# Kernel optimization log

Hardware: AMD Instinct MI355X
Metric: run time of the kernel (lower is better)

Reference implementation:

```python
import itertools
import jax, jax.numpy as jnp
import numpy as np

INIT_STD = 0.1
N_PTS = 1_000_000
PLANE_RES = 512
OUT_DIM = 3
RANK = 8
FEAT_DIM = 32
FEAT_RES = 128


def grid_sample(grid, pts):
    """Equivalent of plenoxels grid_sample_wrapper / torch F.grid_sample.

    grid: [C, *spatial] (d spatial dims, d in {2,3})
    pts:  [N, d] in [-1, 1]; pts[:, k] indexes spatial dim d-1-k (torch x->W, y->H convention)
    bilinear/trilinear interpolation, align_corners=True, zeros padding.
    Returns [N, C].
    """
    spatial = grid.shape[1:]
    d = len(spatial)
    # sizes ordered per-pts-coordinate (reversed spatial order, torch convention)
    sizes_f = jnp.asarray([spatial[d - 1 - k] for k in range(d)], dtype=pts.dtype)
    sizes_i = jnp.asarray([spatial[d - 1 - k] for k in range(d)], dtype=jnp.int32)
    u = (pts + 1.0) * 0.5 * (sizes_f - 1.0)  # unnormalized coords, align_corners=True
    lo = jnp.floor(u)
    frac = u - lo  # [N, d]
    lo = lo.astype(jnp.int32)
    out = jnp.zeros((pts.shape[0], grid.shape[0]), dtype=pts.dtype)
    for corner in itertools.product((0, 1), repeat=d):  # 4 or 8 corners, fixed small loop
        ca = jnp.asarray(corner, dtype=jnp.int32)
        idx = lo + ca  # [N, d]
        valid = jnp.all((idx >= 0) & (idx < sizes_i), axis=-1)  # zeros padding outside
        w = jnp.prod(jnp.where(ca.astype(bool), frac, 1.0 - frac), axis=-1)
        w = w * valid.astype(pts.dtype)
        idx_c = jnp.clip(idx, 0, sizes_i - 1)
        # map pts-coord k back to spatial dim d-1-k for the gather
        vals = grid[(slice(None),) + tuple(idx_c[:, d - 1 - j] for j in range(d))]  # [C, N]
        out = out + w[:, None] * vals.T
    return out


def setup_inputs() -> dict:
    key = jax.random.key(0)
    k1, k2, k3, k4, k5 = jax.random.split(key, 5)
    pts = jax.random.uniform(k1, (N_PTS, 3), minval=-1.0, maxval=1.0, dtype=jnp.float32)
    C = OUT_DIM * RANK
    plane0 = INIT_STD * jax.random.normal(k2, (C, PLANE_RES, PLANE_RES), dtype=jnp.float32)
    plane1 = INIT_STD * jax.random.normal(k3, (C, PLANE_RES, PLANE_RES), dtype=jnp.float32)
    plane2 = INIT_STD * jax.random.normal(k4, (C, PLANE_RES, PLANE_RES), dtype=jnp.float32)
    features = INIT_STD * jax.random.normal(k5, (FEAT_DIM, FEAT_RES, FEAT_RES, FEAT_RES), dtype=jnp.float32)
    return {"pts": pts, "plane0": plane0, "plane1": plane1, "plane2": plane2, "features": features}


def reference(pts, plane0, plane1, plane2, features):
    """LowrankLearnableHash.compute_features: 3 plane bilinear gathers, elementwise
    multiply across planes, sum over rank, then trilinear lookup in feature volume."""
    n = pts.shape[0]
    combs = ((0, 1), (0, 2), (1, 2))  # itertools.combinations(range(3), 2)
    prod = None
    for plane, comb in zip((plane0, plane1, plane2), combs):
        s = grid_sample(plane, pts[:, jnp.asarray(comb)]).reshape(n, OUT_DIM, RANK)
        prod = s if prod is None else prod * s
    interp = prod.sum(axis=-1)  # [N, 3] coordinates into feature volume
    return grid_sample(features, interp)  # [N, FEAT_DIM]
```

## Files before the change

### kernel.cpp

```cpp
#include <hip/hip_runtime.h>

typedef float v4f __attribute__((ext_vector_type(4)));
typedef unsigned short u16;
typedef u16 u16x8 __attribute__((ext_vector_type(8)));

constexpr int PR  = 512;
constexpr int CP  = 24;
constexpr int FD  = 32;
constexpr int FR  = 128;
constexpr int PSZ = PR * PR;
constexpr int NBUCK = 32768;
constexpr int FW  = 16;
constexpr int FW0 = 56;

__device__ inline u16 f2bf(float f) {
    unsigned u = __float_as_uint(f);
    return (u16)((u + 0x7fffu + ((u >> 16) & 1u)) >> 16);
}
__device__ inline float bf2f(u16 h) { return __uint_as_float((unsigned)h << 16); }

__global__ __launch_bounds__(256) void transpose_planes(
    const float* __restrict__ p0, const float* __restrict__ p1,
    const float* __restrict__ p2, u16* __restrict__ wsB)
{
    __shared__ float lds[CP][256];
    int b   = blockIdx.x;
    int p   = b >> 10;
    int rem = b & 1023;
    int y   = rem >> 1;
    int x0  = (rem & 1) << 8;
    const float* src = (p == 0) ? p0 : (p == 1) ? p1 : p2;
    int t = threadIdx.x;
    #pragma unroll
    for (int c = 0; c < CP; ++c)
        lds[c][t] = src[c * PSZ + y * PR + x0 + t];
    __syncthreads();
    int tex = y * PR + x0 + t;
    #pragma unroll
    for (int g = 0; g < 3; ++g) {
        u16x8 w;
        #pragma unroll
        for (int k = 0; k < 8; ++k) w[k] = f2bf(lds[g * 8 + k][t]);
        *(u16x8*)(wsB + ((size_t)(p * 3 + g) * PSZ + tex) * 8) = w;
    }
}

__global__ __launch_bounds__(256) void pack_feat(
    const float* __restrict__ feat, float* __restrict__ wsF)
{
    int t = blockIdx.x * 256 + threadIdx.x;
    int c = t & 31;
    int v = t >> 5;
    int x = v & 15, y = (v >> 4) & 15, z = v >> 8;
    wsF[(size_t)v * FD + c] =
        feat[(size_t)c * FR * FR * FR + (size_t)(z + FW0) * FR * FR
             + (y + FW0) * FR + (x + FW0)];
}

__global__ __launch_bounds__(256) void zero_hist(unsigned* __restrict__ hist)
{
    int t = blockIdx.x * 256 + threadIdx.x;
    v4f z = {0.f, 0.f, 0.f, 0.f};
    *(v4f*)(hist + t * 4) = z;
}

__device__ inline int cell5(float p) {
    int c = (int)floorf((p + 1.0f) * 16.0f);
    return min(max(c, 0), 31);
}
__device__ inline unsigned spread3(unsigned v) {
    return (v & 1u) | ((v & 2u) << 2) | ((v & 4u) << 4) | ((v & 8u) << 6) | ((v & 16u) << 8);
}
__device__ inline unsigned morton_key(float x, float y, float z) {
    return spread3((unsigned)cell5(x)) | (spread3((unsigned)cell5(y)) << 1)
         | (spread3((unsigned)cell5(z)) << 2);
}

__global__ __launch_bounds__(256) void bucket_hist(
    const float* __restrict__ pts, unsigned* __restrict__ hist, int n)
{
    int i = blockIdx.x * blockDim.x + threadIdx.x;
    if (i >= n) return;
    float x = pts[3 * i], y = pts[3 * i + 1], z = pts[3 * i + 2];
    atomicAdd(&hist[morton_key(x, y, z)], 1u);
}

__global__ __launch_bounds__(1024) void scan_offsets(
    const unsigned* __restrict__ hist, unsigned* __restrict__ cursor)
{
    __shared__ unsigned sums[1024];
    int t = threadIdx.x;
    const int base = t * (NBUCK / 1024);
    unsigned loc[NBUCK / 1024];
    unsigned s = 0;
    #pragma unroll
    for (int j = 0; j < NBUCK / 1024; ++j) { loc[j] = s; s += hist[base + j]; }
    sums[t] = s;
    __syncthreads();
    for (int off = 1; off < 1024; off <<= 1) {
        unsigned v = (t >= off) ? sums[t - off] : 0u;
        __syncthreads();
        sums[t] += v;
        __syncthreads();
    }
    unsigned blockbase = (t == 0) ? 0u : sums[t - 1];
    #pragma unroll
    for (int j = 0; j < NBUCK / 1024; ++j) cursor[base + j] = blockbase + loc[j];
}

__global__ __launch_bounds__(256) void scatter_pts(
    const float* __restrict__ pts, unsigned* __restrict__ cursor,
    v4f* __restrict__ sorted, unsigned* __restrict__ ord, int n)
{
    int i = blockIdx.x * blockDim.x + threadIdx.x;
    if (i >= n) return;
    float x = pts[3 * i], y = pts[3 * i + 1], z = pts[3 * i + 2];
    unsigned key = morton_key(x, y, z);
    unsigned pos = atomicAdd(&cursor[key], 1u);
    v4f v; v.x = x; v.y = y; v.z = z; v.w = 0.f;
    sorted[pos] = v;
    ord[pos] = (unsigned)i;
}

template <int G>
__global__ __launch_bounds__(256, 8) void lrh_interp_g(
    const v4f* __restrict__ sorted, const u16* __restrict__ wsB,
    float* __restrict__ itp, int n)
{
    int nwg = gridDim.x;
    int q = nwg >> 3, r = nwg & 7;
    int xcd = blockIdx.x & 7, j = blockIdx.x >> 3;
    int wg = (xcd < r ? xcd * (q + 1) : r * (q + 1) + (xcd - r) * q) + j;
    int i = wg * 256 + threadIdx.x;
    if (i >= n) return;

    v4f pt = __builtin_nontemporal_load(&sorted[i]);
    float cx[3] = {pt.x, pt.x, pt.y};
    float cy[3] = {pt.y, pt.z, pt.z};

    float pr[8] = {1.f, 1.f, 1.f, 1.f, 1.f, 1.f, 1.f, 1.f};
    #pragma unroll
    for (int p = 0; p < 3; ++p) {
        float ux = (cx[p] + 1.0f) * 0.5f * (float)(PR - 1);
        float uy = (cy[p] + 1.0f) * 0.5f * (float)(PR - 1);
        float lx = floorf(ux), ly = floorf(uy);
        float fx = ux - lx,   fy = uy - ly;
        int ix0 = (int)lx, iy0 = (int)ly;
        int ix1 = min(ix0 + 1, PR - 1);
        int iy1 = min(iy0 + 1, PR - 1);
        float wx0 = 1.f - fx, wx1 = fx;
        float wy0 = 1.f - fy, wy1 = fy;
        float w00 = wx0 * wy0, w01 = wx1 * wy0;
        float w10 = wx0 * wy1, w11 = wx1 * wy1;

        const u16* slab = wsB + (size_t)(p * 3 + G) * PSZ * 8;
        const u16x8 A = *(const u16x8*)(slab + (iy0 * PR + ix0) * 8);
        const u16x8 B = *(const u16x8*)(slab + (iy0 * PR + ix1) * 8);
        const u16x8 C = *(const u16x8*)(slab + (iy1 * PR + ix0) * 8);
        const u16x8 D = *(const u16x8*)(slab + (iy1 * PR + ix1) * 8);
        #pragma unroll
        for (int e = 0; e < 8; ++e) {
            float s = w00 * bf2f(A[e]) + w01 * bf2f(B[e])
                    + w10 * bf2f(C[e]) + w11 * bf2f(D[e]);
            pr[e] *= s;
        }
    }
    float itpv = ((pr[0] + pr[1]) + (pr[2] + pr[3]))
               + ((pr[4] + pr[5]) + (pr[6] + pr[7]));
    __builtin_nontemporal_store(itpv, &itp[i]);
}

__global__ __launch_bounds__(256) void lrh_feat(
    const float* __restrict__ itp0, const float* __restrict__ itp1,
    const float* __restrict__ itp2, const unsigned* __restrict__ ord,
    const float* __restrict__ wsF, const float* __restrict__ feat,
    float* __restrict__ out, int n)
{
    int t = blockIdx.x * blockDim.x + threadIdx.x;
    int i = t >> 3, e = t & 7;
    if (i >= n) return;
    float ip[3] = {itp0[i], itp1[i], itp2[i]};
    unsigned orig = ord[i];

    float fr[3];
    int   j0[3];
    bool inw = true;
    #pragma unroll
    for (int k = 0; k < 3; ++k) {
        float uu = (ip[k] + 1.0f) * 0.5f * (float)(FR - 1);
        float lf = floorf(uu);
        fr[k] = uu - lf;
        j0[k] = (int)lf;
        inw = inw && (j0[k] >= FW0) && (j0[k] + 1 <= FW0 + FW - 1);
    }

    v4f r = {0.f, 0.f, 0.f, 0.f};
    if (__builtin_expect(inw, 1)) {
        int lx = j0[0] - FW0, ly = j0[1] - FW0, lz = j0[2] - FW0;
        int base = ((lz * FW + ly) * FW + lx) * FD;
        float wx1 = fr[0], wx0 = 1.f - fr[0];
        float wy1 = fr[1], wy0 = 1.f - fr[1];
        float wz1 = fr[2], wz0 = 1.f - fr[2];
        #pragma unroll
        for (int m = 0; m < 8; ++m) {
            int bx = m & 1, by = (m >> 1) & 1, bz = m >> 2;
            int off = base + (bz * FW * FW + by * FW + bx) * FD;
            float w = (bx ? wx1 : wx0) * (by ? wy1 : wy0) * (bz ? wz1 : wz0);
            v4f f = *(const v4f*)(wsF + off + e * 4);
            #pragma unroll
            for (int c = 0; c < 4; ++c) r[c] = fmaf(w, f[c], r[c]);
        }
    } else {
        float v0[3], v1[3];
        int i0c[3], i1c[3];
        #pragma unroll
        for (int k = 0; k < 3; ++k) {
            int jj = j0[k];
            v0[k] = (jj   >= 0 && jj   < FR) ? 1.f : 0.f;
            v1[k] = (jj+1 >= 0 && jj+1 < FR) ? 1.f : 0.f;
            i0c[k] = min(max(jj,     0), FR - 1);
            i1c[k] = min(max(jj + 1, 0), FR - 1);
        }
        #pragma unroll
        for (int m = 0; m < 8; ++m) {
            int bx = m & 1, by = (m >> 1) & 1, bz = m >> 2;
            int xi = bx ? i1c[0] : i0c[0];
            int yi = by ? i1c[1] : i0c[1];
            int zi = bz ? i1c[2] : i0c[2];
            float w = (bx ? fr[0] * v1[0] : (1.f - fr[0]) * v0[0])
                    * (by ? fr[1] * v1[1] : (1.f - fr[1]) * v0[1])
                    * (bz ? fr[2] * v1[2] : (1.f - fr[2]) * v0[2]);
            int offc = zi * FR * FR + yi * FR + xi;
            #pragma unroll
            for (int c = 0; c < 4; ++c) {
                const float* Fc = feat + (size_t)(e * 4 + c) * (FR * FR * FR);
                r[c] = fmaf(w, Fc[offc], r[c]);
            }
        }
    }

    *(v4f*)(out + (size_t)orig * FD + e * 4) = r;
}

extern "C" void kernel_launch(void* const* d_in, const int* in_sizes, int n_in,
                              void* d_out, int out_size, void* d_ws, size_t ws_size,
                              hipStream_t stream) {
    const float* pts  = (const float*)d_in[0];
    const float* p0   = (const float*)d_in[1];
    const float* p1   = (const float*)d_in[2];
    const float* p2   = (const float*)d_in[3];
    const float* feat = (const float*)d_in[4];
    float* out = (float*)d_out;
    int n = in_sizes[0] / 3;

    size_t off = 0;
    auto alloc = [&](size_t sz) { size_t o = off; off = (off + sz + 255) & ~(size_t)255; return o; };
    const size_t off_trans  = alloc((size_t)3 * PSZ * CP * sizeof(u16));
    const size_t off_sorted = alloc((size_t)n * sizeof(v4f));
    const size_t off_hist   = alloc(NBUCK * sizeof(unsigned));
    const size_t off_cursor = alloc(NBUCK * sizeof(unsigned));
    const size_t off_ord    = alloc((size_t)n * sizeof(unsigned));
    const size_t off_itp0   = alloc((size_t)n * sizeof(float));
    const size_t off_itp1   = alloc((size_t)n * sizeof(float));
    const size_t off_itp2   = alloc((size_t)n * sizeof(float));
    const size_t off_featw  = alloc((size_t)FW * FW * FW * FD * sizeof(float));

    char* ws = (char*)d_ws;
    u16*      wsB     = (u16*)(ws + off_trans);
    v4f*      sorted  = (v4f*)(ws + off_sorted);
    unsigned* hist    = (unsigned*)(ws + off_hist);
    unsigned* cursor  = (unsigned*)(ws + off_cursor);
    unsigned* ord     = (unsigned*)(ws + off_ord);
    float*    itp0    = (float*)(ws + off_itp0);
    float*    itp1    = (float*)(ws + off_itp1);
    float*    itp2    = (float*)(ws + off_itp2);
    float*    wsF     = (float*)(ws + off_featw);

    int blocks = (n + 255) / 256;

    transpose_planes<<<3 * 1024, 256, 0, stream>>>(p0, p1, p2, wsB);
    pack_feat<<<(FW * FW * FW * FD) / 256, 256, 0, stream>>>(feat, wsF);
    zero_hist<<<NBUCK / (256 * 4), 256, 0, stream>>>(hist);
    bucket_hist<<<blocks, 256, 0, stream>>>(pts, hist, n);
    scan_offsets<<<1, 1024, 0, stream>>>(hist, cursor);
    scatter_pts<<<blocks, 256, 0, stream>>>(pts, cursor, sorted, ord, n);
    lrh_interp_g<0><<<blocks, 256, 0, stream>>>(sorted, wsB, itp0, n);
    lrh_interp_g<1><<<blocks, 256, 0, stream>>>(sorted, wsB, itp1, n);
    lrh_interp_g<2><<<blocks, 256, 0, stream>>>(sorted, wsB, itp2, n);
    int fblocks = (int)(((size_t)n * 8 + 255) / 256);
    lrh_feat<<<fblocks, 256, 0, stream>>>(itp0, itp1, itp2, ord, wsF, feat, out, n);
}
```

Measured before the change: 316.2 us.

## Fuse third plane-group interpolation with feature lookup and LDS-staged output scatter

```diff
diff --git a/kernel.cpp b/kernel.cpp
--- a/kernel.cpp
+++ b/kernel.cpp
@@ -12,6 +12,7 @@
 constexpr int NBUCK = 32768;
 constexpr int FW  = 16;
 constexpr int FW0 = 56;
+constexpr int RSTRIDE = 36;
 
 __device__ inline u16 f2bf(float f) {
     unsigned u = __float_as_uint(f);
@@ -110,34 +111,22 @@
 
 __global__ __launch_bounds__(256) void scatter_pts(
     const float* __restrict__ pts, unsigned* __restrict__ cursor,
-    v4f* __restrict__ sorted, unsigned* __restrict__ ord, int n)
+    v4f* __restrict__ sorted, int n)
 {
     int i = blockIdx.x * blockDim.x + threadIdx.x;
     if (i >= n) return;
     float x = pts[3 * i], y = pts[3 * i + 1], z = pts[3 * i + 2];
     unsigned key = morton_key(x, y, z);
     unsigned pos = atomicAdd(&cursor[key], 1u);
-    v4f v; v.x = x; v.y = y; v.z = z; v.w = 0.f;
+    v4f v; v.x = x; v.y = y; v.z = z; v.w = __int_as_float(i);
     sorted[pos] = v;
-    ord[pos] = (unsigned)i;
 }
 
 template <int G>
-__global__ __launch_bounds__(256, 8) void lrh_interp_g(
-    const v4f* __restrict__ sorted, const u16* __restrict__ wsB,
-    float* __restrict__ itp, int n)
-{
-    int nwg = gridDim.x;
-    int q = nwg >> 3, r = nwg & 7;
-    int xcd = blockIdx.x & 7, j = blockIdx.x >> 3;
-    int wg = (xcd < r ? xcd * (q + 1) : r * (q + 1) + (xcd - r) * q) + j;
-    int i = wg * 256 + threadIdx.x;
-    if (i >= n) return;
-
-    v4f pt = __builtin_nontemporal_load(&sorted[i]);
+__device__ inline float interp_group(const v4f pt, const u16* __restrict__ wsB)
+{
     float cx[3] = {pt.x, pt.x, pt.y};
     float cy[3] = {pt.y, pt.z, pt.z};
-
     float pr[8] = {1.f, 1.f, 1.f, 1.f, 1.f, 1.f, 1.f, 1.f};
     #pragma unroll
     for (int p = 0; p < 3; ++p) {
@@ -165,81 +154,136 @@
             pr[e] *= s;
         }
     }
-    float itpv = ((pr[0] + pr[1]) + (pr[2] + pr[3]))
-               + ((pr[4] + pr[5]) + (pr[6] + pr[7]));
-    __builtin_nontemporal_store(itpv, &itp[i]);
-}
-
-__global__ __launch_bounds__(256) void lrh_feat(
+    return ((pr[0] + pr[1]) + (pr[2] + pr[3]))
+         + ((pr[4] + pr[5]) + (pr[6] + pr[7]));
+}
+
+template <int G>
+__global__ __launch_bounds__(256, 8) void lrh_interp_g(
+    const v4f* __restrict__ sorted, const u16* __restrict__ wsB,
+    float* __restrict__ itp, int n)
+{
+    int nwg = gridDim.x;
+    int q = nwg >> 3, r = nwg & 7;
+    int xcd = blockIdx.x & 7, j = blockIdx.x >> 3;
+    int wg = (xcd < r ? xcd * (q + 1) : r * (q + 1) + (xcd - r) * q) + j;
+    int i = wg * 256 + threadIdx.x;
+    if (i >= n) return;
+    v4f pt = __builtin_nontemporal_load(&sorted[i]);
+    float v = interp_group<G>(pt, wsB);
+    __builtin_nontemporal_store(v, &itp[i]);
+}
+
+__global__ __launch_bounds__(256, 4) void lrh_g2_feat(
+    const v4f* __restrict__ sorted, const u16* __restrict__ wsB,
     const float* __restrict__ itp0, const float* __restrict__ itp1,
-    const float* __restrict__ itp2, const unsigned* __restrict__ ord,
     const float* __restrict__ wsF, const float* __restrict__ feat,
     float* __restrict__ out, int n)
 {
-    int t = blockIdx.x * blockDim.x + threadIdx.x;
-    int i = t >> 3, e = t & 7;
-    if (i >= n) return;
-    float ip[3] = {itp0[i], itp1[i], itp2[i]};
-    unsigned orig = ord[i];
-
-    float fr[3];
-    int   j0[3];
-    bool inw = true;
-    #pragma unroll
-    for (int k = 0; k < 3; ++k) {
-        float uu = (ip[k] + 1.0f) * 0.5f * (float)(FR - 1);
-        float lf = floorf(uu);
-        fr[k] = uu - lf;
-        j0[k] = (int)lf;
-        inw = inw && (j0[k] >= FW0) && (j0[k] + 1 <= FW0 + FW - 1);
-    }
-
-    v4f r = {0.f, 0.f, 0.f, 0.f};
-    if (__builtin_expect(inw, 1)) {
-        int lx = j0[0] - FW0, ly = j0[1] - FW0, lz = j0[2] - FW0;
-        int base = ((lz * FW + ly) * FW + lx) * FD;
-        float wx1 = fr[0], wx0 = 1.f - fr[0];
-        float wy1 = fr[1], wy0 = 1.f - fr[1];
-        float wz1 = fr[2], wz0 = 1.f - fr[2];
-        #pragma unroll
-        for (int m = 0; m < 8; ++m) {
-            int bx = m & 1, by = (m >> 1) & 1, bz = m >> 2;
-            int off = base + (bz * FW * FW + by * FW + bx) * FD;
-            float w = (bx ? wx1 : wx0) * (by ? wy1 : wy0) * (bz ? wz1 : wz0);
-            v4f f = *(const v4f*)(wsF + off + e * 4);
-            #pragma unroll
-            for (int c = 0; c < 4; ++c) r[c] = fmaf(w, f[c], r[c]);
-        }
-    } else {
-        float v0[3], v1[3];
-        int i0c[3], i1c[3];
+    __shared__ float rows[256][RSTRIDE];
+    __shared__ unsigned sord[256];
+
+    int nwg = gridDim.x;
+    int q = nwg >> 3, r0 = nwg & 7;
+    int xcd = blockIdx.x & 7, jb = blockIdx.x >> 3;
+    int wg = (xcd < r0 ? xcd * (q + 1) : r0 * (q + 1) + (xcd - r0) * q) + jb;
+    int base = wg * 256;
+    int t = threadIdx.x;
+    int i = base + t;
+
+    if (i < n) {
+        v4f pt = __builtin_nontemporal_load(&sorted[i]);
+        sord[t] = (unsigned)__float_as_int(pt.w);
+        float v2 = interp_group<2>(pt, wsB);
+        float ip[3];
+        ip[0] = __builtin_nontemporal_load(&itp0[i]);
+        ip[1] = __builtin_nontemporal_load(&itp1[i]);
+        ip[2] = v2;
+
+        float fr[3];
+        int   j0[3];
+        bool inw = true;
         #pragma unroll
         for (int k = 0; k < 3; ++k) {
-            int jj = j0[k];
-            v0[k] = (jj   >= 0 && jj   < FR) ? 1.f : 0.f;
-            v1[k] = (jj+1 >= 0 && jj+1 < FR) ? 1.f : 0.f;
-            i0c[k] = min(max(jj,     0), FR - 1);
-            i1c[k] = min(max(jj + 1, 0), FR - 1);
+            float uu = (ip[k] + 1.0f) * 0.5f * (float)(FR - 1);
+            float lf = floorf(uu);
+            fr[k] = uu - lf;
+            j0[k] = (int)lf;
+            inw = inw && (j0[k] >= FW0) && (j0[k] + 1 <= FW0 + FW - 1);
         }
-        #pragma unroll
-        for (int m = 0; m < 8; ++m) {
-            int bx = m & 1, by = (m >> 1) & 1, bz = m >> 2;
-            int xi = bx ? i1c[0] : i0c[0];
-            int yi = by ? i1c[1] : i0c[1];
-            int zi = bz ? i1c[2] : i0c[2];
-            float w = (bx ? fr[0] * v1[0] : (1.f - fr[0]) * v0[0])
-                    * (by ? fr[1] * v1[1] : (1.f - fr[1]) * v0[1])
-                    * (bz ? fr[2] * v1[2] : (1.f - fr[2]) * v0[2]);
-            int offc = zi * FR * FR + yi * FR + xi;
+
+        if (__builtin_expect(inw, 1)) {
+            int lx = j0[0] - FW0, ly = j0[1] - FW0, lz = j0[2] - FW0;
+            const float* cp = wsF + ((lz * FW + ly) * FW + lx) * FD;
+            float wx1 = fr[0], wx0 = 1.f - fr[0];
+            float wy1 = fr[1], wy0 = 1.f - fr[1];
+            float wz1 = fr[2], wz0 = 1.f - fr[2];
+            float wcn[8];
+            int   ofs[8];
             #pragma unroll
-            for (int c = 0; c < 4; ++c) {
-                const float* Fc = feat + (size_t)(e * 4 + c) * (FR * FR * FR);
-                r[c] = fmaf(w, Fc[offc], r[c]);
+            for (int m = 0; m < 8; ++m) {
+                int bx = m & 1, by = (m >> 1) & 1, bz = m >> 2;
+                wcn[m] = (bx ? wx1 : wx0) * (by ? wy1 : wy0) * (bz ? wz1 : wz0);
+                ofs[m] = (bz * FW * FW + by * FW + bx) * FD;
+            }
+            #pragma unroll
+            for (int cg = 0; cg < 8; ++cg) {
+                v4f acc = {0.f, 0.f, 0.f, 0.f};
+                #pragma unroll
+                for (int m = 0; m < 8; ++m) {
+                    v4f f = *(const v4f*)(cp + ofs[m] + cg * 4);
+                    #pragma unroll
+                    for (int c = 0; c < 4; ++c) acc[c] = fmaf(wcn[m], f[c], acc[c]);
+                }
+                *(v4f*)&rows[t][cg * 4] = acc;
+            }
+        } else {
+            float v0[3], v1[3];
+            int i0c[3], i1c[3];
+            #pragma unroll
+            for (int k = 0; k < 3; ++k) {
+                int jj = j0[k];
+                v0[k] = (jj   >= 0 && jj   < FR) ? 1.f : 0.f;
+                v1[k] = (jj+1 >= 0 && jj+1 < FR) ? 1.f : 0.f;
+                i0c[k] = min(max(jj,     0), FR - 1);
+                i1c[k] = min(max(jj + 1, 0), FR - 1);
+            }
+            #pragma unroll
+            for (int cg = 0; cg < 8; ++cg) {
+                v4f acc = {0.f, 0.f, 0.f, 0.f};
+                #pragma unroll
+                for (int m = 0; m < 8; ++m) {
+                    int bx = m & 1, by = (m >> 1) & 1, bz = m >> 2;
+                    int xi = bx ? i1c[0] : i0c[0];
+                    int yi = by ? i1c[1] : i0c[1];
+                    int zi = bz ? i1c[2] : i0c[2];
+                    float w = (bx ? fr[0] * v1[0] : (1.f - fr[0]) * v0[0])
+                            * (by ? fr[1] * v1[1] : (1.f - fr[1]) * v0[1])
+                            * (bz ? fr[2] * v1[2] : (1.f - fr[2]) * v0[2]);
+                    int offc = zi * FR * FR + yi * FR + xi;
+                    #pragma unroll
+                    for (int c = 0; c < 4; ++c) {
+                        const float* Fc = feat + (size_t)(cg * 4 + c) * (FR * FR * FR);
+                        acc[c] = fmaf(w, Fc[offc], acc[c]);
+                    }
+                }
+                *(v4f*)&rows[t][cg * 4] = acc;
             }
         }
     }
-
-    *(v4f*)(out + (size_t)orig * FD + e * 4) = r;
+    __syncthreads();
+
+    int e = t & 7;
+    #pragma unroll
+    for (int rb = 0; rb < 256; rb += 32) {
+        int rr = rb + (t >> 3);
+        if (base + rr < n) {
+            unsigned orow = sord[rr];
+            const float* lp = &rows[rr][e * 4];
+            v4f v = {lp[0], lp[1], lp[2], lp[3]};
+            *(v4f*)(out + (size_t)orow * FD + e * 4) = v;
+        }
+    }
 }
 
 extern "C" void kernel_launch(void* const* d_in, const int* in_sizes, int n_in,
@@ -259,10 +303,8 @@
     const size_t off_sorted = alloc((size_t)n * sizeof(v4f));
     const size_t off_hist   = alloc(NBUCK * sizeof(unsigned));
     const size_t off_cursor = alloc(NBUCK * sizeof(unsigned));
-    const size_t off_ord    = alloc((size_t)n * sizeof(unsigned));
     const size_t off_itp0   = alloc((size_t)n * sizeof(float));
     const size_t off_itp1   = alloc((size_t)n * sizeof(float));
-    const size_t off_itp2   = alloc((size_t)n * sizeof(float));
     const size_t off_featw  = alloc((size_t)FW * FW * FW * FD * sizeof(float));
 
     char* ws = (char*)d_ws;
@@ -270,10 +312,8 @@
     v4f*      sorted  = (v4f*)(ws + off_sorted);
     unsigned* hist    = (unsigned*)(ws + off_hist);
     unsigned* cursor  = (unsigned*)(ws + off_cursor);
-    unsigned* ord     = (unsigned*)(ws + off_ord);
     float*    itp0    = (float*)(ws + off_itp0);
     float*    itp1    = (float*)(ws + off_itp1);
-    float*    itp2    = (float*)(ws + off_itp2);
     float*    wsF     = (float*)(ws + off_featw);
 
     int blocks = (n + 255) / 256;
@@ -283,10 +323,8 @@
     zero_hist<<<NBUCK / (256 * 4), 256, 0, stream>>>(hist);
     bucket_hist<<<blocks, 256, 0, stream>>>(pts, hist, n);
     scan_offsets<<<1, 1024, 0, stream>>>(hist, cursor);
-    scatter_pts<<<blocks, 256, 0, stream>>>(pts, cursor, sorted, ord, n);
+    scatter_pts<<<blocks, 256, 0, stream>>>(pts, cursor, sorted, n);
     lrh_interp_g<0><<<blocks, 256, 0, stream>>>(sorted, wsB, itp0, n);
     lrh_interp_g<1><<<blocks, 256, 0, stream>>>(sorted, wsB, itp1, n);
-    lrh_interp_g<2><<<blocks, 256, 0, stream>>>(sorted, wsB, itp2, n);
-    int fblocks = (int)(((size_t)n * 8 + 255) / 256);
-    lrh_feat<<<fblocks, 256, 0, stream>>>(itp0, itp1, itp2, ord, wsF, feat, out, n);
-}
+    lrh_g2_feat<<<blocks, 256, 0, stream>>>(sorted, wsB, itp0, itp1, wsF, feat, out, n);
+}
```

Measured after the change: 295.0 us. -6.7%, faster.
